# Optimization experiments

Hardware: AMD Instinct MI355X
Metric: run time of the kernel (lower is better)

The kernel has to match this reference:

```python
import jax, jax.numpy as jnp
import numpy as np
from jax import lax


def _conv(x, w, b):
    y = lax.conv_general_dilated(x, w, (1, 1), 'VALID',
                                 dimension_numbers=('NCHW', 'OIHW', 'NCHW'))
    return y + b[None, :, None, None]


def _cubic_weights(t):
    # torch bicubic kernel, A = -0.75
    A = -0.75
    def k1(u):
        return ((A + 2.0) * u - (A + 3.0)) * u * u + 1.0
    def k2(u):
        return ((A * u - 5.0 * A) * u + 8.0 * A) * u - 4.0 * A
    return (k2(t + 1.0), k1(t), k1(1.0 - t), k2(2.0 - t))


def _grid_sample_bicubic(img, grid):
    # img: (N,C,H,W); grid: (N,H,W,2) with (x,y) in [-1,1];
    # align_corners=False, padding_mode='zeros' (torch semantics)
    N, C, H, W = img.shape
    x = ((grid[..., 0] + 1.0) * W - 1.0) * 0.5
    y = ((grid[..., 1] + 1.0) * H - 1.0) * 0.5
    x0 = jnp.floor(x)
    y0 = jnp.floor(y)
    wx = _cubic_weights(x - x0)
    wy = _cubic_weights(y - y0)
    x0i = x0.astype(jnp.int32)
    y0i = y0.astype(jnp.int32)
    flat = img.reshape(N, C, H * W)
    Ho, Wo = x.shape[1], x.shape[2]
    out = jnp.zeros((N, C, Ho, Wo), img.dtype)
    for i in range(4):
        yi = y0i - 1 + i
        vy = (yi >= 0) & (yi < H)
        yic = jnp.clip(yi, 0, H - 1)
        for j in range(4):
            xj = x0i - 1 + j
            valid = vy & (xj >= 0) & (xj < W)
            xjc = jnp.clip(xj, 0, W - 1)
            idx = (yic * W + xjc).reshape(N, 1, Ho * Wo)
            v = jnp.take_along_axis(flat, idx, axis=2).reshape(N, C, Ho, Wo)
            w = jnp.where(valid, wy[i] * wx[j], 0.0)[:, None]
            out = out + v * w
    return out


def _warp_images(disp, images, novelLocation):
    # disp: (N,1,H,W); images: (N,20,H,W); novelLocation: (N,2,H,W)
    N, _, H, W = disp.shape
    d = jnp.moveaxis(disp, 1, -1)                      # (N,H,W,1)
    us = jnp.arange(H, dtype=jnp.float32)
    vs = jnp.arange(W, dtype=jnp.float32)
    gu, gv = jnp.meshgrid(us, vs, indexing='ij')       # torch default indexing
    base = jnp.stack((gu, gv), axis=-1)[None]          # (1,H,W,2) in (row,col)
    q = jnp.moveaxis(novelLocation, 1, -1)             # (N,H,W,2)
    scale = jnp.array([H - 1, W - 1], jnp.float32)
    warped = []
    for i in range(4):
        off = 5 * i
        img = images[:, off:off + 3]
        p = jnp.moveaxis(images[:, off + 3:off + 5], 1, -1)
        loc = base + (p - q) * d                       # (N,H,W,2) (row,col)
        loc = (loc / scale - 0.5) * 2.0
        loc = loc[..., ::-1]                           # flip -> (x=col, y=row)
        warped.append(_grid_sample_bicubic(img, loc))
    return jnp.concatenate(warped + [disp, novelLocation], axis=1)  # (N,15,H,W)


def _disparity_net(x, w1, b1, w2, b2, w3, b3, w4, b4):
    x = jax.nn.relu(_conv(x, w1, b1))
    x = jax.nn.relu(_conv(x, w2, b2))
    x = jax.nn.relu(_conv(x, w3, b3))
    return _conv(x, w4, b4)


def setup_inputs() -> dict:
    key = jax.random.key(0)
    ks = jax.random.split(key, 20)
    inp = {
        'disparityFeatures': jax.random.normal(ks[0], (4, 200, 268, 268), jnp.float32),
        'colorFeatures': jax.random.normal(ks[1], (4, 22, 256, 256), jnp.float32),
    }
    def conv_p(kw, kb, o, c, k):
        fan_in = c * k * k
        w = jax.random.normal(kw, (o, c, k, k), jnp.float32) / np.sqrt(fan_in)
        b = jax.random.normal(kb, (o,), jnp.float32) * 0.01
        return w, b
    inp['dw1'], inp['db1'] = conv_p(ks[2], ks[3], 100, 200, 7)
    inp['dw2'], inp['db2'] = conv_p(ks[4], ks[5], 100, 100, 5)
    inp['dw3'], inp['db3'] = conv_p(ks[6], ks[7], 50, 100, 3)
    inp['dw4'], inp['db4'] = conv_p(ks[8], ks[9], 1, 50, 1)
    inp['cw1'], inp['cb1'] = conv_p(ks[10], ks[11], 100, 15, 7)
    inp['cw2'], inp['cb2'] = conv_p(ks[12], ks[13], 100, 100, 5)
    inp['cw3'], inp['cb3'] = conv_p(ks[14], ks[15], 50, 100, 3)
    inp['cw4'], inp['cb4'] = conv_p(ks[16], ks[17], 3, 50, 1)
    return inp


def reference(disparityFeatures, colorFeatures,
              dw1, db1, dw2, db2, dw3, db3, dw4, db4,
              cw1, cb1, cw2, cb2, cw3, cb3, cw4, cb4):
    images = colorFeatures[:, :-2]
    novelLocation = colorFeatures[:, -2:]
    disparity = _disparity_net(disparityFeatures, dw1, db1, dw2, db2, dw3, db3, dw4, db4)
    warps = _warp_images(disparity, images, novelLocation)
    finalImg = _disparity_net(warps, cw1, cb1, cw2, cb2, cw3, cb3, cw4, cb4)
    return finalImg
```

## Files before the change

kernel.cpp:

```cpp
#include <hip/hip_runtime.h>
#include <cstddef>
#include <cstdint>

typedef _Float16 f16x8 __attribute__((ext_vector_type(8)));
typedef _Float16 f16x4 __attribute__((ext_vector_type(4)));
typedef float    f32x16 __attribute__((ext_vector_type(16)));

__global__ __launch_bounds__(256) void wtrans_kernel(
    const float* __restrict__ w, _Float16* __restrict__ Bt,
    int IC, int OC, int G, int K, int R, int ksteps)
{
    int gid = blockIdx.x * 256 + threadIdx.x;
    if (gid >= ksteps * G * 64) return;
    int ks   = gid / (G * 64);
    int rr   = gid - ks * G * 64;
    int g    = rr >> 6;
    int lane = rr & 63;
    int run = ks % R;
    int t2  = ks / R;
    int ky  = t2 % K;
    int chunk = t2 / K;
    int oc = g * 32 + (lane & 31);
    int kh = lane >> 5;
    _Float16 tmp[8];
    #pragma unroll
    for (int j = 0; j < 8; ++j) {
        int flat = run * 16 + kh * 8 + j;
        int xo  = flat / 20;
        int icl = flat - xo * 20;
        int ic  = chunk * 20 + icl;
        float v = 0.0f;
        if (oc < OC && ic < IC && xo < K)
            v = w[(((size_t)oc * IC + ic) * K + ky) * K + xo];
        tmp[j] = (_Float16)v;
    }
    *(uint4*)(Bt + (size_t)gid * 8) = *(uint4*)tmp;
}

__global__ __launch_bounds__(256) void convin_kernel(
    const float* __restrict__ src, _Float16* __restrict__ dst, int IC)
{
    constexpr int W = 268;
    constexpr int PADS = 272;
    __shared__ float s[20 * PADS];
    int y = blockIdx.x, chunk = blockIdx.y, img = blockIdx.z;
    int tid = threadIdx.x;
    for (int e = tid; e < 20 * W; e += 256) {
        int icl = e / W;
        int x = e - icl * W;
        int ic = chunk * 20 + icl;
        float v = 0.0f;
        if (ic < IC)
            v = src[(((size_t)img * IC + ic) * W + y) * W + x];
        s[icl * PADS + x] = v;
    }
    __syncthreads();
    _Float16* outRow = dst + ((size_t)(img * 10 + chunk) * W + y) * (W * 20);
    for (int u = tid; u < W * 20 / 8; u += 256) {
        _Float16 t[8];
        #pragma unroll
        for (int q = 0; q < 8; ++q) {
            int e = u * 8 + q;
            int px = e / 20;
            int c  = e - px * 20;
            t[q] = (_Float16)s[c * PADS + px];
        }
        *(uint4*)(outRow + (size_t)u * 8) = *(uint4*)t;
    }
}

template<int K, bool RELU>
__global__ __launch_bounds__(256, 3) void conv_mfma(
    const _Float16* __restrict__ in, const _Float16* __restrict__ Bt,
    const float* __restrict__ bias, _Float16* __restrict__ out,
    int Hin, int Win, int OC, int Ho, int Wo,
    int nchunks, int xb, int tilesPerImg, int OG,
    long inStride, long outStride)
{
    constexpr int CB = 20;
    constexpr int R  = (K * CB + 15) / 16;
    constexpr int BM = 8;
    constexpr int PH = BM + K - 1;
    constexpr int MAXF = 31 * CB + R * 16;
    constexpr int PW = (((MAXF + CB - 1) / CB) + 1) & ~1;
    constexpr int ROWF = PW * CB;
    constexpr int UROW = ROWF / 8;
    constexpr int TOT  = PH * UROW;

    __shared__ __align__(16) _Float16 s[PH * ROWF];

    const int tid  = threadIdx.x;
    const int lane = tid & 63;
    const int wm   = tid >> 6;
    const int mcol = lane & 31;
    const int kh   = lane >> 5;
    const int alane = mcol * CB + kh * 8;

    int t = blockIdx.x;
    int img = t / tilesPerImg;
    int rem = t - img * tilesPerImg;
    int og  = rem % OG;
    int tile = rem / OG;
    int byi = tile / xb;
    int bxi = tile - byi * xb;
    int y0 = byi * BM; if (y0 > Ho - BM) y0 = Ho - BM;
    int x0 = bxi * 32; if (x0 > Wo - 32) x0 = Wo - 32;

    const int KSF = OG * 1024;

    const _Float16* inI = in + (size_t)img * inStride;

    f32x16 acc[2][2];
    #pragma unroll
    for (int m = 0; m < 2; ++m)
        #pragma unroll
        for (int n = 0; n < 2; ++n)
            acc[m][n] = (f32x16)(0.0f);

    const int rowE = Win * CB;
    const int mxo  = rowE - 8;
    const size_t chStride = (size_t)Hin * rowE;

    #pragma unroll 1
    for (int chunk = 0; chunk < nchunks; ++chunk) {
        const _Float16* inC = inI + chunk * chStride + (size_t)y0 * rowE;
        #pragma unroll 1
        for (int e = tid; e < TOT; e += 256) {
            int py = e / UROW;
            int uu = e - py * UROW;
            int off = x0 * CB + uu * 8;
            if (off > mxo) off = mxo;
            uint4 val = *(const uint4*)(inC + (size_t)py * rowE + off);
            *(uint4*)&s[(size_t)e * 8] = val;
        }
        __syncthreads();

        const _Float16* BtC = Bt + (size_t)(chunk * K) * R * KSF;
        #pragma unroll 1
        for (int ky = 0; ky < K; ++ky) {
            const _Float16* BtK = BtC + (size_t)(ky * R) * KSF;
            const int rbase = (wm * 2 + ky) * ROWF + alane;
            #pragma unroll
            for (int run = 0; run < R; ++run) {
                const _Float16* bp = BtK + (size_t)run * KSF + og * 1024 + lane * 8;
                f16x8 b0 = *(const f16x8*)bp;
                f16x8 b1 = *(const f16x8*)(bp + 512);
                const int ab = rbase + run * 16;
                #pragma unroll
                for (int mt = 0; mt < 2; ++mt) {
                    const _Float16* ap = &s[ab + mt * ROWF];
                    f16x4 lo = *(const f16x4*)ap;
                    f16x4 hi = *(const f16x4*)(ap + 4);
                    f16x8 a = __builtin_shufflevector(lo, hi, 0, 1, 2, 3, 4, 5, 6, 7);
                    acc[mt][0] = __builtin_amdgcn_mfma_f32_32x32x16_f16(a, b0, acc[mt][0], 0, 0, 0);
                    acc[mt][1] = __builtin_amdgcn_mfma_f32_32x32x16_f16(a, b1, acc[mt][1], 0, 0, 0);
                }
            }
        }
        __syncthreads();
    }

    _Float16* outI = out + (size_t)img * outStride;
    #pragma unroll
    for (int nt = 0; nt < 2; ++nt) {
        int oc = (og * 2 + nt) * 32 + mcol;
        if (oc < OC) {
            float bv = bias[oc];
            int icc = oc / 20;
            int occ = oc - icc * 20;
            _Float16* base = outI + (size_t)icc * Ho * (Wo * 20) + occ;
            #pragma unroll
            for (int mt = 0; mt < 2; ++mt) {
                int y = y0 + wm * 2 + mt;
                _Float16* rowp = base + (size_t)y * (Wo * 20);
                #pragma unroll
                for (int reg = 0; reg < 16; ++reg) {
                    int x = x0 + (reg & 3) + 8 * (reg >> 2) + 4 * kh;
                    float v = acc[mt][nt][reg] + bv;
                    if (RELU) v = fmaxf(v, 0.0f);
                    rowp[(size_t)x * 20] = (_Float16)v;
                }
            }
        }
    }
}

template<int NOUT>
__global__ __launch_bounds__(256) void conv1x1_kernel(
    const _Float16* __restrict__ in, const float* __restrict__ w,
    const float* __restrict__ bias, float* __restrict__ out,
    int N, int IC, long inStride, long outStride)
{
    int px = blockIdx.x * 256 + threadIdx.x;
    int img = blockIdx.y;
    if (px >= N) return;
    const _Float16* p = in + (size_t)img * inStride;
    float a[NOUT];
    #pragma unroll
    for (int o = 0; o < NOUT; ++o) a[o] = 0.0f;
    for (int ic = 0; ic < IC; ++ic) {
        int icc = ic / 20;
        int icl = ic - icc * 20;
        float v = (float)p[((size_t)icc * N + px) * 20 + icl];
        #pragma unroll
        for (int o = 0; o < NOUT; ++o) a[o] = fmaf(v, w[o * IC + ic], a[o]);
    }
    #pragma unroll
    for (int o = 0; o < NOUT; ++o)
        out[(size_t)img * outStride + (size_t)o * N + px] = a[o] + bias[o];
}

__device__ __forceinline__ void cubicw(float t, float w[4])
{
    const float A = -0.75f;
    float u;
    u = t + 1.0f; w[0] = ((A * u - 5.0f * A) * u + 8.0f * A) * u - 4.0f * A;
    u = t;        w[1] = ((A + 2.0f) * u - (A + 3.0f)) * u * u + 1.0f;
    u = 1.0f - t; w[2] = ((A + 2.0f) * u - (A + 3.0f)) * u * u + 1.0f;
    u = 2.0f - t; w[3] = ((A * u - 5.0f * A) * u + 8.0f * A) * u - 4.0f * A;
}

__global__ __launch_bounds__(256) void warp_kernel(
    const float* __restrict__ disp, const float* __restrict__ cf,
    _Float16* __restrict__ outw)
{
    const int P = 65536;
    int idx = blockIdx.x * 256 + threadIdx.x;
    int img = blockIdx.y;
    const float* dI  = disp + (size_t)img * P;
    const float* cfI = cf + (size_t)img * 22 * P;
    _Float16* oI = outw + (size_t)img * 1310720 + (size_t)idx * 20;

    int u = idx >> 8;
    int v = idx & 255;

    float d  = dI[idx];
    float q0 = cfI[20 * P + idx];
    float q1 = cfI[21 * P + idx];

    for (int i = 0; i < 4; ++i) {
        const float* img5 = cfI + (size_t)(5 * i) * P;
        float p0 = img5[3 * P + idx];
        float p1 = img5[4 * P + idx];
        float lr = (float)u + (p0 - q0) * d;
        float lc = (float)v + (p1 - q1) * d;
        float gr = (lr / 255.0f - 0.5f) * 2.0f;
        float gc = (lc / 255.0f - 0.5f) * 2.0f;
        float x = ((gc + 1.0f) * 256.0f - 1.0f) * 0.5f;
        float y = ((gr + 1.0f) * 256.0f - 1.0f) * 0.5f;
        float xf = floorf(x), yf = floorf(y);
        float tx = x - xf, tyy = y - yf;
        float wx[4], wy[4];
        cubicw(tx, wx);
        cubicw(tyy, wy);
        int xi = (int)xf, yi = (int)yf;
        float a0 = 0.f, a1 = 0.f, a2 = 0.f;
        #pragma unroll
        for (int ii = 0; ii < 4; ++ii) {
            int yy = yi - 1 + ii;
            bool vy = (yy >= 0) && (yy < 256);
            int yc = min(max(yy, 0), 255);
            #pragma unroll
            for (int jj = 0; jj < 4; ++jj) {
                int xx = xi - 1 + jj;
                bool vv = vy && (xx >= 0) && (xx < 256);
                int xc = min(max(xx, 0), 255);
                float w = vv ? wy[ii] * wx[jj] : 0.0f;
                int pos = yc * 256 + xc;
                a0 = fmaf(img5[pos], w, a0);
                a1 = fmaf(img5[P + pos], w, a1);
                a2 = fmaf(img5[2 * P + pos], w, a2);
            }
        }
        oI[3 * i + 0] = (_Float16)a0;
        oI[3 * i + 1] = (_Float16)a1;
        oI[3 * i + 2] = (_Float16)a2;
    }
    oI[12] = (_Float16)d;
    oI[13] = (_Float16)q0;
    oI[14] = (_Float16)q1;
    #pragma unroll
    for (int c = 15; c < 20; ++c) oI[c] = (_Float16)0.0f;
}


extern "C" void kernel_launch(void* const* d_in, const int* in_sizes, int n_in,
                              void* d_out, int out_size, void* d_ws, size_t ws_size,
                              hipStream_t stream)
{
    const float* dF  = (const float*)d_in[0];
    const float* cF  = (const float*)d_in[1];
    const float* dw1 = (const float*)d_in[2];
    const float* db1 = (const float*)d_in[3];
    const float* dw2 = (const float*)d_in[4];
    const float* db2 = (const float*)d_in[5];
    const float* dw3 = (const float*)d_in[6];
    const float* db3 = (const float*)d_in[7];
    const float* dw4 = (const float*)d_in[8];
    const float* db4 = (const float*)d_in[9];
    const float* cw1 = (const float*)d_in[10];
    const float* cb1 = (const float*)d_in[11];
    const float* cw2 = (const float*)d_in[12];
    const float* cb2 = (const float*)d_in[13];
    const float* cw3 = (const float*)d_in[14];
    const float* cb3 = (const float*)d_in[15];
    const float* cw4 = (const float*)d_in[16];
    const float* cb4 = (const float*)d_in[17];

    float* outp = (float*)d_out;
    char* ws = (char*)d_ws;

    const size_t O_D1 = 0;
    const size_t O_D2 = O_D1 + 2580480;
    const size_t O_D3 = O_D2 + 716800;
    const size_t O_C1 = O_D3 + 122880;
    const size_t O_C2 = O_C1 + 258048;
    const size_t O_C3 = O_C2 + 716800;
    const size_t O_WEND = O_C3 + 122880;

    _Float16* bt_d1 = (_Float16*)(ws + O_D1);
    _Float16* bt_d2 = (_Float16*)(ws + O_D2);
    _Float16* bt_d3 = (_Float16*)(ws + O_D3);
    _Float16* bt_c1 = (_Float16*)(ws + O_C1);
    _Float16* bt_c2 = (_Float16*)(ws + O_C2);
    _Float16* bt_c3 = (_Float16*)(ws + O_C3);

    auto T = [&](const float* w, _Float16* bt, int IC, int OC, int G,
                 int K, int R, int ksteps) {
        int n = ksteps * G * 64;
        wtrans_kernel<<<(n + 255) / 256, 256, 0, stream>>>(w, bt, IC, OC, G, K, R, ksteps);
    };
    T(dw1, bt_d1, 200, 100, 4, 7, 9, 630);
    T(dw2, bt_d2, 100, 100, 4, 5, 7, 175);
    T(dw3, bt_d3, 100,  50, 2, 3, 4,  60);
    T(cw1, bt_c1,  15, 100, 4, 7, 9,  63);
    T(cw2, bt_c2, 100, 100, 4, 5, 7, 175);
    T(cw3, bt_c3, 100,  50, 2, 3, 4,  60);

    const size_t PER_IMG = (14364800ull + 6864400ull + 6656400ull) * 2;
    int batch = (ws_size >= O_WEND + 4ull * PER_IMG + 1024) ? 4
              : (ws_size >= O_WEND + 2ull * PER_IMG + 1024) ? 2 : 1;

    for (int g0 = 0; g0 < 4; g0 += batch) {
        const int N = batch;
        char* base = ws + O_WEND;
        _Float16* dFc  = (_Float16*)base;
        _Float16* bufA = (_Float16*)(base + 28729600ull * N);
        _Float16* bufB = (_Float16*)(base + (28729600ull + 13728800ull) * N);
        _Float16* bufC = (_Float16*)base;
        float*    disp = (float*)(base + 7864320ull * N);
        _Float16* wrp  = (_Float16*)(base + (7864320ull + 262144ull) * N);

        const float* dFg = dF + (size_t)g0 * 200 * 268 * 268;
        const float* cFg = cF + (size_t)g0 * 22 * 65536;
        float* outg = outp + (size_t)g0 * 3 * 59536;

        convin_kernel<<<dim3(268, 10, N), 256, 0, stream>>>(dFg, dFc, 200);

        conv_mfma<7, true><<<594 * N, 256, 0, stream>>>(
            dFc, bt_d1, db1, bufA, 268, 268, 100, 262, 262, 10, 9, 594, 2,
            14364800L, 6864400L);
        conv_mfma<5, true><<<594 * N, 256, 0, stream>>>(
            bufA, bt_d2, db2, bufB, 262, 262, 100, 258, 258, 5, 9, 594, 2,
            6864400L, 6656400L);
        conv_mfma<3, true><<<256 * N, 256, 0, stream>>>(
            bufB, bt_d3, db3, bufC, 258, 258, 50, 256, 256, 5, 8, 256, 1,
            6656400L, 3932160L);
        conv1x1_kernel<1><<<dim3(256, N), 256, 0, stream>>>(
            bufC, dw4, db4, disp, 65536, 50, 3932160L, 65536L);

        warp_kernel<<<dim3(256, N), 256, 0, stream>>>(disp, cFg, wrp);

        conv_mfma<7, true><<<512 * N, 256, 0, stream>>>(
            wrp, bt_c1, cb1, bufA, 256, 256, 100, 250, 250, 1, 8, 512, 2,
            1310720L, 6250000L);
        conv_mfma<5, true><<<496 * N, 256, 0, stream>>>(
            bufA, bt_c2, cb2, bufB, 250, 250, 100, 246, 246, 5, 8, 496, 2,
            6250000L, 6051600L);
        conv_mfma<3, true><<<248 * N, 256, 0, stream>>>(
            bufB, bt_c3, cb3, bufC, 246, 246, 50, 244, 244, 5, 8, 248, 1,
            6051600L, 3932160L);
        conv1x1_kernel<3><<<dim3(233, N), 256, 0, stream>>>(
            bufC, cw4, cb4, outg, 59536, 50, 3932160L, 178608L);
    }
}
```

Measured before the change: 1.905 ms.

## Cover all output channels per block and reuse A fragments across ky rows

Drops the output-channel-group split, so a block now computes all 4 N-tiles (128 channels) for the 100-channel convs and halves the grid. This stops the input tile being staged into shared memory once per channel group. The loop order becomes run-outer, ky-inner with a rolling two-fragment A buffer, so each shared-memory row fragment is loaded once and used by both M-tiles of adjacent ky. The cost is more accumulator registers (launch bounds drop to 2 blocks per SM for NT=4), fewer blocks, and lower occupancy.

```diff
diff --git a/kernel.cpp b/kernel.cpp
--- a/kernel.cpp
+++ b/kernel.cpp
@@ -69,12 +69,12 @@
     }
 }
 
-template<int K, bool RELU>
-__global__ __launch_bounds__(256, 3) void conv_mfma(
+template<int K, int NT, bool RELU>
+__global__ __launch_bounds__(256, (NT == 4) ? 2 : 3) void conv_mfma(
     const _Float16* __restrict__ in, const _Float16* __restrict__ Bt,
     const float* __restrict__ bias, _Float16* __restrict__ out,
     int Hin, int Win, int OC, int Ho, int Wo,
-    int nchunks, int xb, int tilesPerImg, int OG,
+    int nchunks, int xb, int tilesPerImg,
     long inStride, long outStride)
 {
     constexpr int CB = 20;
@@ -86,6 +86,7 @@
     constexpr int ROWF = PW * CB;
     constexpr int UROW = ROWF / 8;
     constexpr int TOT  = PH * UROW;
+    constexpr int KSF  = NT * 512;
 
     __shared__ __align__(16) _Float16 s[PH * ROWF];
 
@@ -99,22 +100,18 @@
     int t = blockIdx.x;
     int img = t / tilesPerImg;
     int rem = t - img * tilesPerImg;
-    int og  = rem % OG;
-    int tile = rem / OG;
-    int byi = tile / xb;
-    int bxi = tile - byi * xb;
+    int byi = rem / xb;
+    int bxi = rem - byi * xb;
     int y0 = byi * BM; if (y0 > Ho - BM) y0 = Ho - BM;
     int x0 = bxi * 32; if (x0 > Wo - 32) x0 = Wo - 32;
 
-    const int KSF = OG * 1024;
-
     const _Float16* inI = in + (size_t)img * inStride;
 
-    f32x16 acc[2][2];
+    f32x16 acc[2][NT];
     #pragma unroll
     for (int m = 0; m < 2; ++m)
         #pragma unroll
-        for (int n = 0; n < 2; ++n)
+        for (int n = 0; n < NT; ++n)
             acc[m][n] = (f32x16)(0.0f);
 
     const int rowE = Win * CB;
@@ -137,23 +134,35 @@
 
         const _Float16* BtC = Bt + (size_t)(chunk * K) * R * KSF;
         #pragma unroll 1
-        for (int ky = 0; ky < K; ++ky) {
-            const _Float16* BtK = BtC + (size_t)(ky * R) * KSF;
-            const int rbase = (wm * 2 + ky) * ROWF + alane;
+        for (int run = 0; run < R; ++run) {
+            const int abase = alane + run * 16;
+            f16x8 frag[2];
+            {
+                const _Float16* ap = &s[(wm * 2) * ROWF + abase];
+                f16x4 lo = *(const f16x4*)ap;
+                f16x4 hi = *(const f16x4*)(ap + 4);
+                frag[0] = __builtin_shufflevector(lo, hi, 0, 1, 2, 3, 4, 5, 6, 7);
+            }
             #pragma unroll
-            for (int run = 0; run < R; ++run) {
-                const _Float16* bp = BtK + (size_t)run * KSF + og * 1024 + lane * 8;
-                f16x8 b0 = *(const f16x8*)bp;
-                f16x8 b1 = *(const f16x8*)(bp + 512);
-                const int ab = rbase + run * 16;
-                #pragma unroll
-                for (int mt = 0; mt < 2; ++mt) {
-                    const _Float16* ap = &s[ab + mt * ROWF];
+            for (int ky = 0; ky < K; ++ky) {
+                {
+                    const _Float16* ap = &s[(wm * 2 + ky + 1) * ROWF + abase];
                     f16x4 lo = *(const f16x4*)ap;
                     f16x4 hi = *(const f16x4*)(ap + 4);
-                    f16x8 a = __builtin_shufflevector(lo, hi, 0, 1, 2, 3, 4, 5, 6, 7);
-                    acc[mt][0] = __builtin_amdgcn_mfma_f32_32x32x16_f16(a, b0, acc[mt][0], 0, 0, 0);
-                    acc[mt][1] = __builtin_amdgcn_mfma_f32_32x32x16_f16(a, b1, acc[mt][1], 0, 0, 0);
+                    frag[(ky + 1) & 1] =
+                        __builtin_shufflevector(lo, hi, 0, 1, 2, 3, 4, 5, 6, 7);
+                }
+                const _Float16* bp = BtC + (size_t)(ky * R + run) * KSF + lane * 8;
+                f16x8 b[NT];
+                #pragma unroll
+                for (int n = 0; n < NT; ++n)
+                    b[n] = *(const f16x8*)(bp + n * 512);
+                #pragma unroll
+                for (int n = 0; n < NT; ++n) {
+                    acc[0][n] = __builtin_amdgcn_mfma_f32_32x32x16_f16(
+                        frag[ky & 1], b[n], acc[0][n], 0, 0, 0);
+                    acc[1][n] = __builtin_amdgcn_mfma_f32_32x32x16_f16(
+                        frag[(ky + 1) & 1], b[n], acc[1][n], 0, 0, 0);
                 }
             }
         }
@@ -162,8 +171,8 @@
 
     _Float16* outI = out + (size_t)img * outStride;
     #pragma unroll
-    for (int nt = 0; nt < 2; ++nt) {
-        int oc = (og * 2 + nt) * 32 + mcol;
+    for (int nt = 0; nt < NT; ++nt) {
+        int oc = nt * 32 + mcol;
         if (oc < OC) {
             float bv = bias[oc];
             int icc = oc / 20;
@@ -357,28 +366,28 @@
 
         convin_kernel<<<dim3(268, 10, N), 256, 0, stream>>>(dFg, dFc, 200);
 
-        conv_mfma<7, true><<<594 * N, 256, 0, stream>>>(
-            dFc, bt_d1, db1, bufA, 268, 268, 100, 262, 262, 10, 9, 594, 2,
+        conv_mfma<7, 4, true><<<297 * N, 256, 0, stream>>>(
+            dFc, bt_d1, db1, bufA, 268, 268, 100, 262, 262, 10, 9, 297,
             14364800L, 6864400L);
-        conv_mfma<5, true><<<594 * N, 256, 0, stream>>>(
-            bufA, bt_d2, db2, bufB, 262, 262, 100, 258, 258, 5, 9, 594, 2,
+        conv_mfma<5, 4, true><<<297 * N, 256, 0, stream>>>(
+            bufA, bt_d2, db2, bufB, 262, 262, 100, 258, 258, 5, 9, 297,
             6864400L, 6656400L);
-        conv_mfma<3, true><<<256 * N, 256, 0, stream>>>(
-            bufB, bt_d3, db3, bufC, 258, 258, 50, 256, 256, 5, 8, 256, 1,
+        conv_mfma<3, 2, true><<<256 * N, 256, 0, stream>>>(
+            bufB, bt_d3, db3, bufC, 258, 258, 50, 256, 256, 5, 8, 256,
             6656400L, 3932160L);
         conv1x1_kernel<1><<<dim3(256, N), 256, 0, stream>>>(
             bufC, dw4, db4, disp, 65536, 50, 3932160L, 65536L);
 
         warp_kernel<<<dim3(256, N), 256, 0, stream>>>(disp, cFg, wrp);
 
-        conv_mfma<7, true><<<512 * N, 256, 0, stream>>>(
-            wrp, bt_c1, cb1, bufA, 256, 256, 100, 250, 250, 1, 8, 512, 2,
+        conv_mfma<7, 4, true><<<256 * N, 256, 0, stream>>>(
+            wrp, bt_c1, cb1, bufA, 256, 256, 100, 250, 250, 1, 8, 256,
             1310720L, 6250000L);
-        conv_mfma<5, true><<<496 * N, 256, 0, stream>>>(
-            bufA, bt_c2, cb2, bufB, 250, 250, 100, 246, 246, 5, 8, 496, 2,
+        conv_mfma<5, 4, true><<<248 * N, 256, 0, stream>>>(
+            bufA, bt_c2, cb2, bufB, 250, 250, 100, 246, 246, 5, 8, 248,
             6250000L, 6051600L);
-        conv_mfma<3, true><<<248 * N, 256, 0, stream>>>(
-            bufB, bt_c3, cb3, bufC, 246, 246, 50, 244, 244, 5, 8, 248, 1,
+        conv_mfma<3, 2, true><<<248 * N, 256, 0, stream>>>(
+            bufB, bt_c3, cb3, bufC, 246, 246, 50, 244, 244, 5, 8, 248,
             6051600L, 3932160L);
         conv1x1_kernel<3><<<dim3(233, N), 256, 0, stream>>>(
             bufC, cw4, cb4, outg, 59536, 50, 3932160L, 178608L);
```

After: 2.196 ms. 15.3% more time.
